# Performance work log

Hardware: AMD Instinct MI355X
Metric: run time of the kernel (lower is better)

Reference implementation:

```python
import jax, jax.numpy as jnp
import numpy as np

N, E, NNZ, CIN, COUT = 100000, 25000, 1600000, 256, 256


def setup_inputs() -> dict:
    key = jax.random.key(0)
    k_x, k_v, k_e, k_w = jax.random.split(key, 4)
    X = jax.random.normal(k_x, (N, CIN), dtype=jnp.float32)
    v_idx = jax.random.randint(k_v, (NNZ,), 0, N)      # vertex of each incidence pair
    e_idx = jax.random.randint(k_e, (NNZ,), 0, E)      # hyperedge of each incidence pair
    # kaiming_normal_ on theta.weight: std = sqrt(2 / fan_in)
    W = jax.random.normal(k_w, (CIN, COUT), dtype=jnp.float32) * np.sqrt(2.0 / CIN)
    b = jnp.zeros((COUT,), dtype=jnp.float32)
    return {"X": X, "W": W, "b": b, "v_idx": v_idx, "e_idx": e_idx}


def reference(X, W, b, v_idx, e_idx):
    # theta: linear projection
    Xp = X @ W + b  # [N, COUT]

    # degrees (edge weights = 1)
    ones = jnp.ones((NNZ,), dtype=Xp.dtype)
    dv = jax.ops.segment_sum(ones, v_idx, num_segments=N)  # vertex degree
    de = jax.ops.segment_sum(ones, e_idx, num_segments=E)  # hyperedge degree
    dv_isqrt = jnp.where(dv > 0, jax.lax.rsqrt(jnp.maximum(dv, 1.0)), 0.0)
    de_inv = jnp.where(de > 0, 1.0 / jnp.maximum(de, 1.0), 0.0)

    # smoothing_with_HGNN: D_v^{-1/2} H D_e^{-1} H^T D_v^{-1/2} Xp
    Xs = Xp * dv_isqrt[:, None]                                            # [N, C]
    Ye = jax.ops.segment_sum(Xs[v_idx], e_idx, num_segments=E) * de_inv[:, None]  # [E, C]
    Zv = jax.ops.segment_sum(Ye[e_idx], v_idx, num_segments=N) * dv_isqrt[:, None]  # [N, C]

    # not is_last: ReLU; bn is None (use_bn=False); dropout identity at eval
    return jax.nn.relu(Zv)
```

## Files before the change

kernel.cpp:

```cpp
#include <hip/hip_runtime.h>
#include <hip/hip_bf16.h>

#define NV 100000
#define NE 25000
#define NNZ_ 1600000
#define CH 256
#define ESTRIDE 128
#define VSTRIDE 48
#define LDSK 264

typedef unsigned int u32;
typedef unsigned short u16;
typedef __attribute__((ext_vector_type(8))) short bf16x8;
typedef __attribute__((ext_vector_type(4))) float f32x4;

__device__ __forceinline__ float bf2f(u16 u){ return __uint_as_float(((u32)u)<<16); }
__device__ __forceinline__ u16 f2bf(float f){ __hip_bfloat16 h = __float2bfloat16(f); return *reinterpret_cast<u16*>(&h); }
__device__ __forceinline__ void acc4(float4& a, ushort4 u){
  a.x += bf2f(u.x); a.y += bf2f(u.y); a.z += bf2f(u.z); a.w += bf2f(u.w);
}

__global__ void k_build(const int* __restrict__ v_idx, const int* __restrict__ e_idx,
                        int* __restrict__ dv_cnt, int* __restrict__ de_cnt,
                        u16* __restrict__ v_listP, int* __restrict__ e_listP){
  int part = blockIdx.x & 7;
  int grp  = blockIdx.x >> 3;
  int ngrp = gridDim.x >> 3;
  int eLo = part*(NE/8), eHi = eLo + (NE/8);
  int vLo = part*(NV/8), vHi = vLo + (NV/8);
  int i = grp*blockDim.x + threadIdx.x;
  int stride = ngrp*blockDim.x;
  for (; i<NNZ_; i+=stride){
    int v = __builtin_nontemporal_load(&v_idx[i]);
    int e = __builtin_nontemporal_load(&e_idx[i]);
    if (e>=eLo && e<eHi){ int s = atomicAdd(&de_cnt[e],1); e_listP[(e<<7)+s] = v; }
    if (v>=vLo && v<vHi){ int s = atomicAdd(&dv_cnt[v],1); v_listP[v*VSTRIDE+s] = (u16)e; }
  }
}

__global__ void k_dvis(const int* __restrict__ dv_cnt, float* __restrict__ dv_isqrt){
  int v = blockIdx.x*blockDim.x + threadIdx.x;
  if (v < NV){ int d = dv_cnt[v]; dv_isqrt[v] = d>0 ? rsqrtf((float)d) : 0.f; }
}

__global__ void k_xs(const float4* __restrict__ X4, const float* __restrict__ dv_isqrt,
                     ushort4* __restrict__ Xs4){
  int i = blockIdx.x*blockDim.x + threadIdx.x;
  int v = i >> 6;
  float w = dv_isqrt[v];
  float4 x = X4[i];
  ushort4 o;
  o.x = f2bf(x.x*w); o.y = f2bf(x.y*w); o.z = f2bf(x.z*w); o.w = f2bf(x.w*w);
  Xs4[i] = o;
}

__global__ void k_wh(const float* __restrict__ W, u16* __restrict__ Wh){
  __shared__ float tile[16][17];
  int bx=blockIdx.x, by=blockIdx.y;
  int tx=threadIdx.x, ty=threadIdx.y;
  tile[ty][tx] = W[(by*16+ty)*256 + bx*16+tx];
  __syncthreads();
  Wh[(bx*16+ty)*256 + by*16+tx] = f2bf(tile[tx][ty]);
}

__global__ __launch_bounds__(256) void k_tegemm(const int* __restrict__ de_cnt,
                     const int* __restrict__ e_listP, const ushort4* __restrict__ Xs4,
                     const float* __restrict__ dv_isqrt, const u16* __restrict__ Wh,
                     float* __restrict__ tb, u16* __restrict__ Ue){
  __shared__ u16 lds[16][LDSK];
  int t = threadIdx.x, w = t>>6, lane = t&63;
  int e0 = blockIdx.x*16;

  for (int j=0;j<4;++j){
    int e = e0 + w*4 + j;
    int r = w*4 + j;
    float4 a0=make_float4(0,0,0,0), a1=make_float4(0,0,0,0);
    float ts = 0.f;
    if (e < NE){
      int deg = de_cnt[e], base = e<<7;
      int m = 0;
      for (; m+8 <= deg; m += 8){
        int v0=e_listP[base+m+0], v1=e_listP[base+m+1], v2=e_listP[base+m+2], v3=e_listP[base+m+3];
        int v4=e_listP[base+m+4], v5=e_listP[base+m+5], v6=e_listP[base+m+6], v7=e_listP[base+m+7];
        ushort4 u0=Xs4[(v0<<6)+lane], u1=Xs4[(v1<<6)+lane], u2=Xs4[(v2<<6)+lane], u3=Xs4[(v3<<6)+lane];
        ushort4 u4=Xs4[(v4<<6)+lane], u5=Xs4[(v5<<6)+lane], u6=Xs4[(v6<<6)+lane], u7=Xs4[(v7<<6)+lane];
        acc4(a0,u0); acc4(a1,u1); acc4(a0,u2); acc4(a1,u3);
        acc4(a0,u4); acc4(a1,u5); acc4(a0,u6); acc4(a1,u7);
        ts += dv_isqrt[v0]+dv_isqrt[v1]+dv_isqrt[v2]+dv_isqrt[v3]
            + dv_isqrt[v4]+dv_isqrt[v5]+dv_isqrt[v6]+dv_isqrt[v7];
      }
      for (; m<deg; ++m){
        int v = e_listP[base+m];
        ushort4 u = Xs4[(v<<6)+lane];
        acc4(a0,u);
        ts += dv_isqrt[v];
      }
      float dinv = deg>0 ? 1.f/(float)deg : 0.f;
      a0.x=(a0.x+a1.x)*dinv; a0.y=(a0.y+a1.y)*dinv; a0.z=(a0.z+a1.z)*dinv; a0.w=(a0.w+a1.w)*dinv;
      if (lane==0) tb[e] = ts*dinv;
    }
    ushort4 o;
    o.x=f2bf(a0.x); o.y=f2bf(a0.y); o.z=f2bf(a0.z); o.w=f2bf(a0.w);
    *reinterpret_cast<ushort4*>(&lds[r][lane*4]) = o;
  }
  __syncthreads();

  int rr = lane & 15, kg = lane >> 4;
  f32x4 acc0={0,0,0,0}, acc1={0,0,0,0}, acc2={0,0,0,0}, acc3={0,0,0,0};
  #pragma unroll
  for (int s=0; s<8; ++s){
    bf16x8 a = *reinterpret_cast<bf16x8*>(&lds[rr][s*32 + kg*8]);
    const u16* wb = &Wh[(size_t)((w*4)*16 + rr)*256 + s*32 + kg*8];
    bf16x8 b0 = *reinterpret_cast<const bf16x8*>(wb);
    bf16x8 b1 = *reinterpret_cast<const bf16x8*>(wb + 16*256);
    bf16x8 b2 = *reinterpret_cast<const bf16x8*>(wb + 32*256);
    bf16x8 b3 = *reinterpret_cast<const bf16x8*>(wb + 48*256);
    acc0 = __builtin_amdgcn_mfma_f32_16x16x32_bf16(a, b0, acc0, 0,0,0);
    acc1 = __builtin_amdgcn_mfma_f32_16x16x32_bf16(a, b1, acc1, 0,0,0);
    acc2 = __builtin_amdgcn_mfma_f32_16x16x32_bf16(a, b2, acc2, 0,0,0);
    acc3 = __builtin_amdgcn_mfma_f32_16x16x32_bf16(a, b3, acc3, 0,0,0);
  }
  __syncthreads();
  #pragma unroll
  for (int reg=0; reg<4; ++reg){
    int row = kg*4 + reg;
    lds[row][(w*4+0)*16 + rr] = f2bf(acc0[reg]);
    lds[row][(w*4+1)*16 + rr] = f2bf(acc1[reg]);
    lds[row][(w*4+2)*16 + rr] = f2bf(acc2[reg]);
    lds[row][(w*4+3)*16 + rr] = f2bf(acc3[reg]);
  }
  __syncthreads();
  int orow = t>>4, oseg = t&15;
  int e = e0 + orow;
  if (e < NE){
    uint4 d0 = *reinterpret_cast<uint4*>(&lds[orow][oseg*16]);
    uint4 d1 = *reinterpret_cast<uint4*>(&lds[orow][oseg*16+8]);
    *reinterpret_cast<uint4*>(&Ue[(size_t)e*256 + oseg*16])     = d0;
    *reinterpret_cast<uint4*>(&Ue[(size_t)e*256 + oseg*16 + 8]) = d1;
  }
}

__global__ __launch_bounds__(256) void k_zv(const int* __restrict__ dv_cnt, const u16* __restrict__ v_listP,
                    const ushort4* __restrict__ Ue4, const float* __restrict__ tb,
                    const float* __restrict__ dv_isqrt, const float4* __restrict__ b4,
                    float4* __restrict__ out4){
  int v = blockIdx.x*4 + (threadIdx.x>>6);
  if (v >= NV) return;
  int lane = threadIdx.x & 63;
  int deg = dv_cnt[v];
  int base = v*VSTRIDE;
  float4 a0 = make_float4(0,0,0,0), a1 = make_float4(0,0,0,0);
  float sb0 = 0.f, sb1 = 0.f;
  int m = 0;
  for (; m+8 <= deg; m += 8){
    int e0=v_listP[base+m+0], e1=v_listP[base+m+1], e2=v_listP[base+m+2], e3=v_listP[base+m+3];
    int e4=v_listP[base+m+4], e5=v_listP[base+m+5], e6=v_listP[base+m+6], e7=v_listP[base+m+7];
    ushort4 u0=Ue4[(e0<<6)+lane], u1=Ue4[(e1<<6)+lane], u2=Ue4[(e2<<6)+lane], u3=Ue4[(e3<<6)+lane];
    ushort4 u4=Ue4[(e4<<6)+lane], u5=Ue4[(e5<<6)+lane], u6=Ue4[(e6<<6)+lane], u7=Ue4[(e7<<6)+lane];
    acc4(a0,u0); acc4(a1,u1); acc4(a0,u2); acc4(a1,u3);
    acc4(a0,u4); acc4(a1,u5); acc4(a0,u6); acc4(a1,u7);
    sb0 += tb[e0]+tb[e2]+tb[e4]+tb[e6];
    sb1 += tb[e1]+tb[e3]+tb[e5]+tb[e7];
  }
  for (; m<deg; ++m){
    int e = v_listP[base+m];
    ushort4 u = Ue4[(e<<6)+lane];
    acc4(a0,u);
    sb0 += tb[e];
  }
  float4 acc;
  acc.x=a0.x+a1.x; acc.y=a0.y+a1.y; acc.z=a0.z+a1.z; acc.w=a0.w+a1.w;
  float w = dv_isqrt[v];
  float sw = (sb0+sb1)*w;
  float4 bb = b4[lane];
  float4 o;
  o.x = fmaxf(0.f, fmaf(sw, bb.x, acc.x*w));
  o.y = fmaxf(0.f, fmaf(sw, bb.y, acc.y*w));
  o.z = fmaxf(0.f, fmaf(sw, bb.z, acc.z*w));
  o.w = fmaxf(0.f, fmaf(sw, bb.w, acc.w*w));
  out4[(v<<6)+lane] = o;
}

extern "C" void kernel_launch(void* const* d_in, const int* in_sizes, int n_in,
                              void* d_out, int out_size, void* d_ws, size_t ws_size,
                              hipStream_t stream) {
  const float* X = (const float*)d_in[0];
  const float* W = (const float*)d_in[1];
  const float* b = (const float*)d_in[2];
  const int* v_idx = (const int*)d_in[3];
  const int* e_idx = (const int*)d_in[4];
  float* out = (float*)d_out;

  char* p = (char*)d_ws;
  auto alloc = [&](size_t bytes)->void*{
    void* r = (void*)p; p += (bytes + 255) & ~(size_t)255; return r;
  };
  int* dv_cnt     = (int*)alloc((size_t)NV*4);
  int* de_cnt     = (int*)alloc((size_t)NE*4);
  float* dv_isqrt = (float*)alloc((size_t)NV*4);
  float* tb       = (float*)alloc((size_t)NE*4);
  int* e_listP    = (int*)alloc((size_t)NE*ESTRIDE*4);
  u16* v_listP    = (u16*)alloc((size_t)NV*VSTRIDE*2);
  u16* Wh         = (u16*)alloc((size_t)CH*CH*2);
  u16* Ue         = (u16*)alloc((size_t)NE*CH*2);
  u16* Xs         = (u16*)d_out;

  hipMemsetAsync(dv_cnt, 0, (size_t)NV*4, stream);
  hipMemsetAsync(de_cnt, 0, (size_t)NE*4, stream);

  k_build<<<1024,256,0,stream>>>(v_idx,e_idx,dv_cnt,de_cnt,v_listP,e_listP);
  k_dvis<<<(NV+255)/256,256,0,stream>>>(dv_cnt, dv_isqrt);
  k_xs<<<(NV*64)/256,256,0,stream>>>((const float4*)X, dv_isqrt, (ushort4*)Xs);
  k_wh<<<dim3(16,16),dim3(16,16),0,stream>>>(W, Wh);
  k_tegemm<<<(NE+15)/16,256,0,stream>>>(de_cnt,e_listP,(const ushort4*)Xs,dv_isqrt,Wh,tb,Ue);
  k_zv<<<(NV+3)/4,256,0,stream>>>(dv_cnt,v_listP,(const ushort4*)Ue,tb,dv_isqrt,(const float4*)b,(float4*)out);
}
```

Measured before the change: 437.1 us.

## Replace atomic padded adjacency build with two-level bucketed counting sort into CSR

Replaces the single atomic-append build into fixed-stride padded lists with a deterministic CSR construction. It runs a per-tile bin histogram, a multi-kernel prefix scan, a scatter into coarse bins, and a per-bin LDS counting sort that produces e_off/e_list and v_off/v_list. This removes the scattered global atomics, the eight-way redundant index passes, and the fixed-capacity padding. Lists become compact, and overflow beyond the old strides is no longer possible. The cost is about ten extra small kernel launches and extra passes over the NNZ indices plus temporary buffers, with Ue aliased onto tmpE.

```diff
diff --git a/kernel.cpp b/kernel.cpp
--- a/kernel.cpp
+++ b/kernel.cpp
@@ -5,8 +5,12 @@
 #define NE 25000
 #define NNZ_ 1600000
 #define CH 256
-#define ESTRIDE 128
-#define VSTRIDE 48
+#define TS 4096
+#define NB_T 391
+#define EBINS 196
+#define VBINS 196
+#define HTOT (196*NB_T)
+#define SEGCAP 9216
 #define LDSK 264
 
 typedef unsigned int u32;
@@ -20,27 +24,161 @@
   a.x += bf2f(u.x); a.y += bf2f(u.y); a.z += bf2f(u.z); a.w += bf2f(u.w);
 }
 
-__global__ void k_build(const int* __restrict__ v_idx, const int* __restrict__ e_idx,
-                        int* __restrict__ dv_cnt, int* __restrict__ de_cnt,
-                        u16* __restrict__ v_listP, int* __restrict__ e_listP){
-  int part = blockIdx.x & 7;
-  int grp  = blockIdx.x >> 3;
-  int ngrp = gridDim.x >> 3;
-  int eLo = part*(NE/8), eHi = eLo + (NE/8);
-  int vLo = part*(NV/8), vHi = vLo + (NV/8);
-  int i = grp*blockDim.x + threadIdx.x;
-  int stride = ngrp*blockDim.x;
-  for (; i<NNZ_; i+=stride){
-    int v = __builtin_nontemporal_load(&v_idx[i]);
-    int e = __builtin_nontemporal_load(&e_idx[i]);
-    if (e>=eLo && e<eHi){ int s = atomicAdd(&de_cnt[e],1); e_listP[(e<<7)+s] = v; }
-    if (v>=vLo && v<vHi){ int s = atomicAdd(&dv_cnt[v],1); v_listP[v*VSTRIDE+s] = (u16)e; }
-  }
-}
-
-__global__ void k_dvis(const int* __restrict__ dv_cnt, float* __restrict__ dv_isqrt){
+__global__ __launch_bounds__(256) void k_hist(const int* __restrict__ v_idx, const int* __restrict__ e_idx,
+                       int* __restrict__ histE, int* __restrict__ histV){
+  __shared__ int hE[EBINS], hV[VBINS];
+  for (int i=threadIdx.x;i<EBINS;i+=256) hE[i]=0;
+  for (int i=threadIdx.x;i<VBINS;i+=256) hV[i]=0;
+  __syncthreads();
+  int i0 = blockIdx.x*TS;
+  int n = min(TS, NNZ_-i0);
+  for (int k=threadIdx.x;k<n;k+=256){
+    int e = e_idx[i0+k], v = v_idx[i0+k];
+    atomicAdd(&hE[e>>7],1);
+    atomicAdd(&hV[v>>9],1);
+  }
+  __syncthreads();
+  for (int i=threadIdx.x;i<EBINS;i+=256) histE[i*NB_T+blockIdx.x]=hE[i];
+  for (int i=threadIdx.x;i<VBINS;i+=256) histV[i*NB_T+blockIdx.x]=hV[i];
+}
+
+__global__ void k_scanA(const int* cnt, int n, int* off, int* bsum){
+  __shared__ int buf[1024];
+  int i = blockIdx.x*1024 + threadIdx.x;
+  int x = (i<n) ? cnt[i] : 0;
+  buf[threadIdx.x] = x;
+  __syncthreads();
+  #pragma unroll
+  for (int d=1; d<1024; d<<=1){
+    int t = (threadIdx.x>=d) ? buf[threadIdx.x-d] : 0;
+    __syncthreads();
+    buf[threadIdx.x] += t;
+    __syncthreads();
+  }
+  if (i<n) off[i] = buf[threadIdx.x] - x;
+  if (threadIdx.x==1023) bsum[blockIdx.x] = buf[1023];
+}
+
+__global__ void k_scanB(int* bsum, int nb){
+  __shared__ int buf[128];
+  int x = (threadIdx.x<nb) ? bsum[threadIdx.x] : 0;
+  buf[threadIdx.x] = x;
+  __syncthreads();
+  #pragma unroll
+  for (int d=1; d<128; d<<=1){
+    int t = (threadIdx.x>=d) ? buf[threadIdx.x-d] : 0;
+    __syncthreads();
+    buf[threadIdx.x] += t;
+    __syncthreads();
+  }
+  if (threadIdx.x<nb) bsum[threadIdx.x] = buf[threadIdx.x] - x;
+}
+
+__global__ void k_scanC2(int* off, const int* __restrict__ bsum, int n){
+  int i = blockIdx.x*blockDim.x + threadIdx.x;
+  if (i<n) off[i] += bsum[i>>10];
+}
+
+__global__ __launch_bounds__(256) void k_scat(const int* __restrict__ v_idx, const int* __restrict__ e_idx,
+                       const int* __restrict__ baseE, const int* __restrict__ baseV,
+                       u32* __restrict__ tmpE, u32* __restrict__ tmpV){
+  __shared__ int bE[EBINS], bV[VBINS], cE[EBINS], cV[VBINS];
+  for (int i=threadIdx.x;i<EBINS;i+=256){ bE[i]=baseE[i*NB_T+blockIdx.x]; cE[i]=0; }
+  for (int i=threadIdx.x;i<VBINS;i+=256){ bV[i]=baseV[i*NB_T+blockIdx.x]; cV[i]=0; }
+  __syncthreads();
+  int i0 = blockIdx.x*TS;
+  int n = min(TS, NNZ_-i0);
+  for (int k=threadIdx.x;k<n;k+=256){
+    int e = e_idx[i0+k], v = v_idx[i0+k];
+    int be = e>>7, bv = v>>9;
+    int r  = atomicAdd(&cE[be],1);
+    tmpE[bE[be]+r] = ((u32)e<<17) | (u32)v;
+    int r2 = atomicAdd(&cV[bv],1);
+    tmpV[bV[bv]+r2] = ((u32)v<<15) | (u32)e;
+  }
+}
+
+__global__ __launch_bounds__(256) void k_seg2e(const int* __restrict__ baseE, const u32* __restrict__ tmpE,
+                        int* __restrict__ e_off, int* __restrict__ e_list){
+  int seg = blockIdx.x;
+  int s0 = baseE[seg*NB_T];
+  int s1 = (seg+1<EBINS) ? baseE[(seg+1)*NB_T] : NNZ_;
+  int len = s1 - s0;
+  __shared__ u32 buf[SEGCAP];
+  __shared__ int cnt[128], st[129];
+  for (int i=threadIdx.x;i<128;i+=256) cnt[i]=0;
+  __syncthreads();
+  bool fit = (len <= SEGCAP);
+  if (fit){
+    for (int i=threadIdx.x;i<len;i+=256){ u32 p=tmpE[s0+i]; buf[i]=p; atomicAdd(&cnt[(p>>17)&127],1); }
+  } else {
+    for (int i=threadIdx.x;i<len;i+=256){ u32 p=tmpE[s0+i]; atomicAdd(&cnt[(p>>17)&127],1); }
+  }
+  __syncthreads();
+  if (threadIdx.x==0){ int a=0; for (int i=0;i<128;i++){ st[i]=a; a+=cnt[i]; } st[128]=a; }
+  __syncthreads();
+  for (int i=threadIdx.x;i<128;i+=256){
+    int e = seg*128 + i;
+    if (e < NE) e_off[e] = s0 + st[i];
+  }
+  if (seg==EBINS-1 && threadIdx.x==0) e_off[NE] = NNZ_;
+  for (int i=threadIdx.x;i<128;i+=256) cnt[i]=0;
+  __syncthreads();
+  if (fit){
+    for (int i=threadIdx.x;i<len;i+=256){
+      u32 p=buf[i]; int lb=(p>>17)&127; int r=atomicAdd(&cnt[lb],1);
+      e_list[s0+st[lb]+r] = (int)(p & 0x1FFFFu);
+    }
+  } else {
+    for (int i=threadIdx.x;i<len;i+=256){
+      u32 p=tmpE[s0+i]; int lb=(p>>17)&127; int r=atomicAdd(&cnt[lb],1);
+      e_list[s0+st[lb]+r] = (int)(p & 0x1FFFFu);
+    }
+  }
+}
+
+__global__ __launch_bounds__(256) void k_seg2v(const int* __restrict__ baseV, const u32* __restrict__ tmpV,
+                        int* __restrict__ v_off, u16* __restrict__ v_list){
+  int seg = blockIdx.x;
+  int s0 = baseV[seg*NB_T];
+  int s1 = (seg+1<VBINS) ? baseV[(seg+1)*NB_T] : NNZ_;
+  int len = s1 - s0;
+  __shared__ u32 buf[SEGCAP];
+  __shared__ int cnt[512], st[513];
+  for (int i=threadIdx.x;i<512;i+=256) cnt[i]=0;
+  __syncthreads();
+  bool fit = (len <= SEGCAP);
+  if (fit){
+    for (int i=threadIdx.x;i<len;i+=256){ u32 p=tmpV[s0+i]; buf[i]=p; atomicAdd(&cnt[(p>>15)&511],1); }
+  } else {
+    for (int i=threadIdx.x;i<len;i+=256){ u32 p=tmpV[s0+i]; atomicAdd(&cnt[(p>>15)&511],1); }
+  }
+  __syncthreads();
+  if (threadIdx.x==0){ int a=0; for (int i=0;i<512;i++){ st[i]=a; a+=cnt[i]; } st[512]=a; }
+  __syncthreads();
+  for (int i=threadIdx.x;i<512;i+=256){
+    int v = seg*512 + i;
+    if (v < NV) v_off[v] = s0 + st[i];
+  }
+  if (seg==VBINS-1 && threadIdx.x==0) v_off[NV] = NNZ_;
+  for (int i=threadIdx.x;i<512;i+=256) cnt[i]=0;
+  __syncthreads();
+  if (fit){
+    for (int i=threadIdx.x;i<len;i+=256){
+      u32 p=buf[i]; int lb=(p>>15)&511; int r=atomicAdd(&cnt[lb],1);
+      v_list[s0+st[lb]+r] = (u16)(p & 0x7FFFu);
+    }
+  } else {
+    for (int i=threadIdx.x;i<len;i+=256){
+      u32 p=tmpV[s0+i]; int lb=(p>>15)&511; int r=atomicAdd(&cnt[lb],1);
+      v_list[s0+st[lb]+r] = (u16)(p & 0x7FFFu);
+    }
+  }
+}
+
+__global__ void k_dvis(const int* __restrict__ v_off, float* __restrict__ dv_isqrt){
   int v = blockIdx.x*blockDim.x + threadIdx.x;
-  if (v < NV){ int d = dv_cnt[v]; dv_isqrt[v] = d>0 ? rsqrtf((float)d) : 0.f; }
+  if (v < NV){ int d = v_off[v+1]-v_off[v]; dv_isqrt[v] = d>0 ? rsqrtf((float)d) : 0.f; }
 }
 
 __global__ void k_xs(const float4* __restrict__ X4, const float* __restrict__ dv_isqrt,
@@ -63,8 +201,8 @@
   Wh[(bx*16+ty)*256 + by*16+tx] = f2bf(tile[tx][ty]);
 }
 
-__global__ __launch_bounds__(256) void k_tegemm(const int* __restrict__ de_cnt,
-                     const int* __restrict__ e_listP, const ushort4* __restrict__ Xs4,
+__global__ __launch_bounds__(256) void k_tegemm(const int* __restrict__ e_off,
+                     const int* __restrict__ e_list, const ushort4* __restrict__ Xs4,
                      const float* __restrict__ dv_isqrt, const u16* __restrict__ Wh,
                      float* __restrict__ tb, u16* __restrict__ Ue){
   __shared__ u16 lds[16][LDSK];
@@ -77,11 +215,11 @@
     float4 a0=make_float4(0,0,0,0), a1=make_float4(0,0,0,0);
     float ts = 0.f;
     if (e < NE){
-      int deg = de_cnt[e], base = e<<7;
+      int beg = e_off[e], deg = e_off[e+1]-beg;
       int m = 0;
       for (; m+8 <= deg; m += 8){
-        int v0=e_listP[base+m+0], v1=e_listP[base+m+1], v2=e_listP[base+m+2], v3=e_listP[base+m+3];
-        int v4=e_listP[base+m+4], v5=e_listP[base+m+5], v6=e_listP[base+m+6], v7=e_listP[base+m+7];
+        int v0=e_list[beg+m+0], v1=e_list[beg+m+1], v2=e_list[beg+m+2], v3=e_list[beg+m+3];
+        int v4=e_list[beg+m+4], v5=e_list[beg+m+5], v6=e_list[beg+m+6], v7=e_list[beg+m+7];
         ushort4 u0=Xs4[(v0<<6)+lane], u1=Xs4[(v1<<6)+lane], u2=Xs4[(v2<<6)+lane], u3=Xs4[(v3<<6)+lane];
         ushort4 u4=Xs4[(v4<<6)+lane], u5=Xs4[(v5<<6)+lane], u6=Xs4[(v6<<6)+lane], u7=Xs4[(v7<<6)+lane];
         acc4(a0,u0); acc4(a1,u1); acc4(a0,u2); acc4(a1,u3);
@@ -90,7 +228,7 @@
             + dv_isqrt[v4]+dv_isqrt[v5]+dv_isqrt[v6]+dv_isqrt[v7];
       }
       for (; m<deg; ++m){
-        int v = e_listP[base+m];
+        int v = e_list[beg+m];
         ushort4 u = Xs4[(v<<6)+lane];
         acc4(a0,u);
         ts += dv_isqrt[v];
@@ -140,21 +278,21 @@
   }
 }
 
-__global__ __launch_bounds__(256) void k_zv(const int* __restrict__ dv_cnt, const u16* __restrict__ v_listP,
+__global__ __launch_bounds__(256) void k_zv(const int* __restrict__ v_off, const u16* __restrict__ v_list,
                     const ushort4* __restrict__ Ue4, const float* __restrict__ tb,
                     const float* __restrict__ dv_isqrt, const float4* __restrict__ b4,
                     float4* __restrict__ out4){
   int v = blockIdx.x*4 + (threadIdx.x>>6);
   if (v >= NV) return;
   int lane = threadIdx.x & 63;
-  int deg = dv_cnt[v];
-  int base = v*VSTRIDE;
+  int base = v_off[v];
+  int deg = v_off[v+1] - base;
   float4 a0 = make_float4(0,0,0,0), a1 = make_float4(0,0,0,0);
   float sb0 = 0.f, sb1 = 0.f;
   int m = 0;
   for (; m+8 <= deg; m += 8){
-    int e0=v_listP[base+m+0], e1=v_listP[base+m+1], e2=v_listP[base+m+2], e3=v_listP[base+m+3];
-    int e4=v_listP[base+m+4], e5=v_listP[base+m+5], e6=v_listP[base+m+6], e7=v_listP[base+m+7];
+    int e0=v_list[base+m+0], e1=v_list[base+m+1], e2=v_list[base+m+2], e3=v_list[base+m+3];
+    int e4=v_list[base+m+4], e5=v_list[base+m+5], e6=v_list[base+m+6], e7=v_list[base+m+7];
     ushort4 u0=Ue4[(e0<<6)+lane], u1=Ue4[(e1<<6)+lane], u2=Ue4[(e2<<6)+lane], u3=Ue4[(e3<<6)+lane];
     ushort4 u4=Ue4[(e4<<6)+lane], u5=Ue4[(e5<<6)+lane], u6=Ue4[(e6<<6)+lane], u7=Ue4[(e7<<6)+lane];
     acc4(a0,u0); acc4(a1,u1); acc4(a0,u2); acc4(a1,u3);
@@ -163,7 +301,7 @@
     sb1 += tb[e1]+tb[e3]+tb[e5]+tb[e7];
   }
   for (; m<deg; ++m){
-    int e = v_listP[base+m];
+    int e = v_list[base+m];
     ushort4 u = Ue4[(e<<6)+lane];
     acc4(a0,u);
     sb0 += tb[e];
@@ -195,23 +333,38 @@
   auto alloc = [&](size_t bytes)->void*{
     void* r = (void*)p; p += (bytes + 255) & ~(size_t)255; return r;
   };
-  int* dv_cnt     = (int*)alloc((size_t)NV*4);
-  int* de_cnt     = (int*)alloc((size_t)NE*4);
+  int* histE      = (int*)alloc((size_t)HTOT*4);
+  int* histV      = (int*)alloc((size_t)HTOT*4);
+  int* bsumE      = (int*)alloc(128*4);
+  int* bsumV      = (int*)alloc(128*4);
+  int* e_off      = (int*)alloc((size_t)(NE+1)*4);
+  int* v_off      = (int*)alloc((size_t)(NV+1)*4);
   float* dv_isqrt = (float*)alloc((size_t)NV*4);
   float* tb       = (float*)alloc((size_t)NE*4);
-  int* e_listP    = (int*)alloc((size_t)NE*ESTRIDE*4);
-  u16* v_listP    = (u16*)alloc((size_t)NV*VSTRIDE*2);
+  u32* tmpE       = (u32*)alloc((size_t)NNZ_*4);
+  u32* tmpV       = (u32*)alloc((size_t)NNZ_*4);
+  int* e_list     = (int*)alloc((size_t)NNZ_*4);
+  u16* v_list     = (u16*)alloc((size_t)NNZ_*2);
   u16* Wh         = (u16*)alloc((size_t)CH*CH*2);
-  u16* Ue         = (u16*)alloc((size_t)NE*CH*2);
+  u16* Ue         = (u16*)tmpE;
   u16* Xs         = (u16*)d_out;
 
-  hipMemsetAsync(dv_cnt, 0, (size_t)NV*4, stream);
-  hipMemsetAsync(de_cnt, 0, (size_t)NE*4, stream);
-
-  k_build<<<1024,256,0,stream>>>(v_idx,e_idx,dv_cnt,de_cnt,v_listP,e_listP);
-  k_dvis<<<(NV+255)/256,256,0,stream>>>(dv_cnt, dv_isqrt);
+  const int nbS = (HTOT+1023)/1024;
+
+  k_hist<<<NB_T,256,0,stream>>>(v_idx,e_idx,histE,histV);
+  k_scanA<<<nbS,1024,0,stream>>>(histE,HTOT,histE,bsumE);
+  k_scanA<<<nbS,1024,0,stream>>>(histV,HTOT,histV,bsumV);
+  k_scanB<<<1,128,0,stream>>>(bsumE,nbS);
+  k_scanB<<<1,128,0,stream>>>(bsumV,nbS);
+  k_scanC2<<<(HTOT+255)/256,256,0,stream>>>(histE,bsumE,HTOT);
+  k_scanC2<<<(HTOT+255)/256,256,0,stream>>>(histV,bsumV,HTOT);
+  k_scat<<<NB_T,256,0,stream>>>(v_idx,e_idx,histE,histV,tmpE,tmpV);
+  k_seg2e<<<EBINS,256,0,stream>>>(histE,tmpE,e_off,e_list);
+  k_seg2v<<<VBINS,256,0,stream>>>(histV,tmpV,v_off,v_list);
+
+  k_dvis<<<(NV+255)/256,256,0,stream>>>(v_off, dv_isqrt);
   k_xs<<<(NV*64)/256,256,0,stream>>>((const float4*)X, dv_isqrt, (ushort4*)Xs);
   k_wh<<<dim3(16,16),dim3(16,16),0,stream>>>(W, Wh);
-  k_tegemm<<<(NE+15)/16,256,0,stream>>>(de_cnt,e_listP,(const ushort4*)Xs,dv_isqrt,Wh,tb,Ue);
-  k_zv<<<(NV+3)/4,256,0,stream>>>(dv_cnt,v_listP,(const ushort4*)Ue,tb,dv_isqrt,(const float4*)b,(float4*)out);
-}
+  k_tegemm<<<(NE+15)/16,256,0,stream>>>(e_off,e_list,(const ushort4*)Xs,dv_isqrt,Wh,tb,Ue);
+  k_zv<<<(NV+3)/4,256,0,stream>>>(v_off,v_list,(const ushort4*)Ue,tb,dv_isqrt,(const float4*)b,(float4*)out);
+}
```

After: 369.7 us. 15.4% less time.
